# Optimization experiments

Hardware: AMD Instinct MI355X
Metric: run time of the kernel (lower is better)

Reference implementation:

```python
import jax, jax.numpy as jnp
import numpy as np

D_MODEL = 1024
H = 16
D_K = D_MODEL // H
D_FF = 4096
EPS = 1e-6
NEG = -1.0e9


def setup_inputs() -> dict:
    key = jax.random.key(0)
    ks = jax.random.split(key, 8)
    B, S = 4, 2048
    x = jax.random.normal(ks[0], (B, S, D_MODEL), dtype=jnp.float32)
    src_mask = jnp.ones((B, 1, S, S), dtype=jnp.int32)
    s = 0.02
    wq = jax.random.normal(ks[1], (D_MODEL, D_MODEL), jnp.float32) * s
    wk = jax.random.normal(ks[2], (D_MODEL, D_MODEL), jnp.float32) * s
    wv = jax.random.normal(ks[3], (D_MODEL, D_MODEL), jnp.float32) * s
    wo = jax.random.normal(ks[4], (D_MODEL, D_MODEL), jnp.float32) * s
    w1 = jax.random.normal(ks[5], (D_MODEL, D_FF), jnp.float32) * s
    b1 = jnp.zeros((D_FF,), jnp.float32)
    w2 = jax.random.normal(ks[6], (D_FF, D_MODEL), jnp.float32) * s
    b2 = jnp.zeros((D_MODEL,), jnp.float32)
    # LayerNorm params are scalars in the original (torch.ones(1)/zeros(1))
    a1 = jnp.ones((1,), jnp.float32); bt1 = jnp.zeros((1,), jnp.float32)
    a2 = jnp.ones((1,), jnp.float32); bt2 = jnp.zeros((1,), jnp.float32)
    return {"x": x, "src_mask": src_mask, "wq": wq, "wk": wk, "wv": wv,
            "wo": wo, "w1": w1, "b1": b1, "w2": w2, "b2": b2,
            "a1": a1, "bt1": bt1, "a2": a2, "bt2": bt2}


def _layernorm(x, alpha, beta):
    # Original: (x - mean) / (std + eps), std with Bessel correction (torch default)
    mean = jnp.mean(x, axis=-1, keepdims=True)
    std = jnp.std(x, axis=-1, keepdims=True, ddof=1)
    return alpha * (x - mean) / (std + EPS) + beta


def _mha(x, mask, wq, wk, wv, wo):
    B, S, _ = x.shape
    q = (x @ wq).reshape(B, S, H, D_K).transpose(0, 2, 1, 3)  # [B,H,S,Dk]
    k = (x @ wk).reshape(B, S, H, D_K).transpose(0, 2, 1, 3)
    v = (x @ wv).reshape(B, S, H, D_K).transpose(0, 2, 1, 3)
    scores = jnp.einsum('bhqd,bhkd->bhqk', q, k) / jnp.sqrt(jnp.float32(D_K))
    scores = jnp.where(mask == 0, NEG, scores)
    attn = jax.nn.softmax(scores, axis=-1)
    out = jnp.einsum('bhqk,bhkd->bhqd', attn, v)  # [B,H,S,Dk]
    out = out.transpose(0, 2, 1, 3).reshape(B, S, D_MODEL)
    return out @ wo


def reference(x, src_mask, wq, wk, wv, wo, w1, b1, w2, b2, a1, bt1, a2, bt2):
    # Sublayer 1: self-attention with post-norm residual (dropout = eval/identity)
    attn_out = _mha(x, src_mask, wq, wk, wv, wo)
    x = _layernorm(x + attn_out, a1, bt1)
    # Sublayer 2: FFN with post-norm residual
    ffn_out = jax.nn.relu(x @ w1 + b1) @ w2 + b2
    x = _layernorm(x + ffn_out, a2, bt2)
    return x
```

## Files before the change

### kernel.cpp

```cpp
#include <hip/hip_runtime.h>
#include <stdint.h>

typedef __bf16 bf16x8 __attribute__((ext_vector_type(8)));
typedef float f32x4 __attribute__((ext_vector_type(4)));
typedef unsigned short u16;
typedef u16 u16x8 __attribute__((ext_vector_type(8)));
typedef u16 u16x4 __attribute__((ext_vector_type(4)));
typedef uint32_t u32;

#define DEV __device__ __forceinline__
#define MFMA(a, b, c) __builtin_amdgcn_mfma_f32_16x16x32_bf16(a, b, c, 0, 0, 0)

static constexpr int B_ = 4, S_ = 2048, M_ = 8192, D_ = 1024, H_ = 16, DFF_ = 4096;

DEV u16 f2bf(float f) {
    union { float f; u32 u; } c; c.f = f;
    u32 u = c.u;
    return (u16)((u + 0x7fffu + ((u >> 16) & 1u)) >> 16);
}

DEV u32 cvt_pk_bf16(float lo, float hi) {
    u32 r;
    asm("v_cvt_pk_bf16_f32 %0, %1, %2" : "=v"(r) : "v"(lo), "v"(hi));
    return r;
}

DEV float v_exp2(float x) {
    float r;
    asm("v_exp_f32 %0, %1" : "=v"(r) : "v"(x));
    return r;
}

DEV void gload16(void* lds, const void* g) {
    __builtin_amdgcn_global_load_lds(
        (const __attribute__((address_space(1))) unsigned int*)g,
        (__attribute__((address_space(3))) unsigned int*)lds, 16, 0, 0);
}


__global__ __launch_bounds__(256) void k_pack_mask(const int* __restrict__ m,
                                                   u32* __restrict__ bits, int nwords) {
    int w = blockIdx.x * 256 + threadIdx.x;
    if (w >= nwords) return;
    const int4* s = (const int4*)(m + (size_t)w * 32);
    u32 r = 0;
#pragma unroll
    for (int j = 0; j < 8; j++) {
        int4 v = s[j];
        r |= (u32)(v.x != 0) << (j * 4) | (u32)(v.y != 0) << (j * 4 + 1) |
             (u32)(v.z != 0) << (j * 4 + 2) | (u32)(v.w != 0) << (j * 4 + 3);
    }
    bits[w] = r;
}

__global__ __launch_bounds__(256) void k_cast_bf16(const float* __restrict__ s,
                                                   u16* __restrict__ d, int n4) {
    int i = blockIdx.x * 256 + threadIdx.x;
    if (i >= n4) return;
    f32x4 v = ((const f32x4*)s)[i];
    u16x4 o;
    o[0] = f2bf(v[0]); o[1] = f2bf(v[1]); o[2] = f2bf(v[2]); o[3] = f2bf(v[3]);
    ((u16x4*)d)[i] = o;
}

__global__ void k_transpose_cast(const float* __restrict__ s, u16* __restrict__ d,
                                 int K, int N) {
    __shared__ float t[32][33];
    int n0 = blockIdx.x * 32, k0 = blockIdx.y * 32;
    int tx = threadIdx.x, ty = threadIdx.y;
#pragma unroll
    for (int i = 0; i < 4; i++)
        t[ty + i * 8][tx] = s[(size_t)(k0 + ty + i * 8) * N + n0 + tx];
    __syncthreads();
#pragma unroll
    for (int i = 0; i < 4; i++)
        d[(size_t)(n0 + ty + i * 8) * K + k0 + tx] = f2bf(t[tx][ty + i * 8]);
}

template <int EPI>
__global__ __launch_bounds__(512, 4) void k_gemm8(const u16* __restrict__ A,
                                                  const u16* __restrict__ Bt,
                                                  float* __restrict__ Cf,
                                                  u16* __restrict__ Cb,
                                                  const float* __restrict__ bias,
                                                  const float* __restrict__ resid,
                                                  u16* __restrict__ Vt,
                                                  int N, int K) {
    __shared__ u16 As[2][128 * 64];
    __shared__ u16 Bs[2][128 * 64];
    const int tid = threadIdx.x, lane = tid & 63, wave = tid >> 6;
    const int lr = lane & 15, lg = lane >> 4;
    const int wm = wave >> 1, wn = wave & 1;
    const int nbx = N >> 7;
    const int chunk = gridDim.x >> 3;
    const int id = ((int)blockIdx.x & 7) * chunk + ((int)blockIdx.x >> 3);
    const size_t row0 = (size_t)(id / nbx) * 128;
    const int col0 = (id % nbx) * 128;
    const int srow = lane >> 3;
    const int sgr = (lane & 7) ^ srow;
    const int NT = K >> 6;
    f32x4 acc[2][4] = {};

    auto stage = [&](int buf, int t) {
#pragma unroll
        for (int i = 0; i < 2; i++) {
            int c = i * 8 + wave;
            gload16((char*)&As[buf][0] + c * 1024,
                    (const char*)(A + (row0 + c * 8 + srow) * K + t * 64 + sgr * 8));
        }
#pragma unroll
        for (int i = 0; i < 2; i++) {
            int c = i * 8 + wave;
            gload16((char*)&Bs[buf][0] + c * 1024,
                    (const char*)(Bt + (size_t)(col0 + c * 8 + srow) * K + t * 64 + sgr * 8));
        }
    };

    stage(0, 0);
    for (int t = 0; t < NT; ++t) {
        const int cur = t & 1;
        if (t + 1 < NT) {
            stage(cur ^ 1, t + 1);
            asm volatile("s_waitcnt vmcnt(4)" ::: "memory");
        } else {
            asm volatile("s_waitcnt vmcnt(0)" ::: "memory");
        }
        __builtin_amdgcn_s_barrier();
        asm volatile("" ::: "memory");
        bf16x8 bF[4][2];
#pragma unroll
        for (int n = 0; n < 4; n++) {
            int r = wn * 64 + n * 16 + lr;
            int rb = r * 128, sw = (r & 7) << 4;
#pragma unroll
            for (int ks = 0; ks < 2; ks++)
                bF[n][ks] = *(const bf16x8*)((char*)&Bs[cur][0] +
                                             (rb + ((ks * 64 + lg * 16) ^ sw)));
        }
#pragma unroll
        for (int m = 0; m < 2; m++) {
            int r = wm * 32 + m * 16 + lr;
            int rb = r * 128, sw = (r & 7) << 4;
            bf16x8 a0 = *(const bf16x8*)((char*)&As[cur][0] + (rb + ((lg * 16) ^ sw)));
            bf16x8 a1 = *(const bf16x8*)((char*)&As[cur][0] + (rb + ((64 + lg * 16) ^ sw)));
            __builtin_amdgcn_s_setprio(1);
#pragma unroll
            for (int n = 0; n < 4; n++) {
                acc[m][n] = MFMA(a0, bF[n][0], acc[m][n]);
                acc[m][n] = MFMA(a1, bF[n][1], acc[m][n]);
            }
            __builtin_amdgcn_s_setprio(0);
        }
        asm volatile("" ::: "memory");
        __builtin_amdgcn_s_barrier();
    }
#pragma unroll
    for (int m = 0; m < 2; m++)
#pragma unroll
        for (int n = 0; n < 4; n++) {
            const int cg = col0 + wn * 64 + n * 16 + lr;
            const int rbase = (int)row0 + wm * 32 + m * 16 + lg * 4;
            if constexpr (EPI == 0) {
                const int proj = cg >> 10, hh = (cg >> 6) & 15, dk = cg & 63;
                const int b = rbase >> 11, s = rbase & 2047;
                if (proj == 2) {
                    u16x4 ov;
#pragma unroll
                    for (int i = 0; i < 4; i++) ov[i] = f2bf(acc[m][n][i]);
                    *(u16x4*)(Vt + ((size_t)(b * 16 + hh) * 64 + dk) * 2048 + s) = ov;
                } else {
                    const float sc = (proj == 0) ? 0.1803368801111832f : 1.f;
                    size_t base = ((size_t)(proj * 64 + b * 16 + hh) * 2048 + s) * 64 + dk;
#pragma unroll
                    for (int i = 0; i < 4; i++)
                        Cb[base + (size_t)i * 64] = f2bf(acc[m][n][i] * sc);
                }
            } else {
#pragma unroll
                for (int i = 0; i < 4; i++) {
                    const int rg = rbase + i;
                    float v = acc[m][n][i];
                    if constexpr (EPI == 1) {
                        Cf[(size_t)rg * N + cg] = v + resid[(size_t)rg * N + cg];
                    } else if constexpr (EPI == 2) {
                        v += bias[cg];
                        v = v > 0.f ? v : 0.f;
                        Cb[(size_t)rg * N + cg] = f2bf(v);
                    } else {
                        Cf[(size_t)rg * N + cg] = v + bias[cg] + resid[(size_t)rg * N + cg];
                    }
                }
            }
        }
}

template <int EPI>
__global__ __launch_bounds__(512, 2) void k_gemm256(const u16* __restrict__ A,
                                                    const u16* __restrict__ Bt,
                                                    float* __restrict__ Cf,
                                                    u16* __restrict__ Cb,
                                                    const float* __restrict__ bias,
                                                    int N, int K) {
    __shared__ u16 As[2][256 * 64];
    __shared__ u16 Bs[2][256 * 64];
    const int tid = threadIdx.x, lane = tid & 63, wave = tid >> 6;
    const int lr = lane & 15, lg = lane >> 4;
    const int wm = wave >> 2, wn = wave & 3;
    const int nbx = N >> 8;
    const int chunk = gridDim.x >> 3;
    const int id = ((int)blockIdx.x & 7) * chunk + ((int)blockIdx.x >> 3);
    const size_t row0 = (size_t)(id / nbx) * 256;
    const int col0 = (id % nbx) * 256;
    const int srow = lane >> 3;
    const int sgr = (lane & 7) ^ srow;
    const int NT = K >> 6;
    f32x4 acc[8][4] = {};

    auto stage_half = [&](int isB, int buf, int t, int h) {
        const u16* g = isB ? Bt : A;
        const size_t grow0 = isB ? (size_t)col0 : row0;
        char* base = isB ? (char*)&Bs[buf][0] : (char*)&As[buf][0];
#pragma unroll
        for (int l = 0; l < 2; l++) {
            int rt = h * 128 + l * 64 + wave * 8;
            gload16(base + rt * 128,
                    (const char*)(g + (grow0 + rt + srow) * K + t * 64 + sgr * 8));
        }
    };
    auto rdA = [&](int cur, int mh, int m, int kk) -> bf16x8 {
        int r = wm * 128 + mh * 64 + m * 16 + lr;
        int gi = kk * 4 + lg;
        return *(const bf16x8*)((char*)&As[cur][0] + r * 128 + ((gi ^ (r & 7)) << 4));
    };
    auto rdB = [&](int cur, int nh, int n, int kk) -> bf16x8 {
        int r = wn * 64 + nh * 32 + n * 16 + lr;
        int gi = kk * 4 + lg;
        return *(const bf16x8*)((char*)&Bs[cur][0] + r * 128 + ((gi ^ (r & 7)) << 4));
    };

    stage_half(0, 0, 0, 0); stage_half(0, 0, 0, 1);
    stage_half(1, 0, 0, 0); stage_half(1, 0, 0, 1);
    stage_half(1, 1, 1, 0); stage_half(1, 1, 1, 1);
    asm volatile("s_waitcnt vmcnt(4)" ::: "memory");
    __builtin_amdgcn_s_barrier();

    bf16x8 aF[4][2], b0F[2][2], b1F[2][2];
    for (int t = 0; t < NT; ++t) {
        const int cur = t & 1, nxt = cur ^ 1;
#pragma unroll
        for (int m = 0; m < 4; m++) { aF[m][0] = rdA(cur, 0, m, 0); aF[m][1] = rdA(cur, 0, m, 1); }
#pragma unroll
        for (int n = 0; n < 2; n++) { b0F[n][0] = rdB(cur, 0, n, 0); b0F[n][1] = rdB(cur, 0, n, 1); }
        if (t + 1 < NT) stage_half(0, nxt, t + 1, 0);
        __builtin_amdgcn_s_barrier();
        asm volatile("s_waitcnt lgkmcnt(0)" ::: "memory");
        __builtin_amdgcn_sched_barrier(0);
        __builtin_amdgcn_s_setprio(1);
#pragma unroll
        for (int m = 0; m < 4; m++)
#pragma unroll
            for (int n = 0; n < 2; n++) {
                acc[m][n] = MFMA(aF[m][0], b0F[n][0], acc[m][n]);
                acc[m][n] = MFMA(aF[m][1], b0F[n][1], acc[m][n]);
            }
        __builtin_amdgcn_s_setprio(0);
        __builtin_amdgcn_s_barrier();
#pragma unroll
        for (int n = 0; n < 2; n++) { b1F[n][0] = rdB(cur, 1, n, 0); b1F[n][1] = rdB(cur, 1, n, 1); }
        if (t + 1 < NT) stage_half(0, nxt, t + 1, 1);
        __builtin_amdgcn_s_barrier();
        asm volatile("s_waitcnt lgkmcnt(0)" ::: "memory");
        __builtin_amdgcn_sched_barrier(0);
        __builtin_amdgcn_s_setprio(1);
#pragma unroll
        for (int m = 0; m < 4; m++)
#pragma unroll
            for (int n = 0; n < 2; n++) {
                acc[m][2 + n] = MFMA(aF[m][0], b1F[n][0], acc[m][2 + n]);
                acc[m][2 + n] = MFMA(aF[m][1], b1F[n][1], acc[m][2 + n]);
            }
        __builtin_amdgcn_s_setprio(0);
        __builtin_amdgcn_s_barrier();
#pragma unroll
        for (int m = 0; m < 4; m++) { aF[m][0] = rdA(cur, 1, m, 0); aF[m][1] = rdA(cur, 1, m, 1); }
        if (t + 2 < NT) stage_half(1, cur, t + 2, 0);
        __builtin_amdgcn_s_barrier();
        asm volatile("s_waitcnt lgkmcnt(0)" ::: "memory");
        __builtin_amdgcn_sched_barrier(0);
        __builtin_amdgcn_s_setprio(1);
#pragma unroll
        for (int m = 0; m < 4; m++)
#pragma unroll
            for (int n = 0; n < 2; n++) {
                acc[4 + m][2 + n] = MFMA(aF[m][0], b1F[n][0], acc[4 + m][2 + n]);
                acc[4 + m][2 + n] = MFMA(aF[m][1], b1F[n][1], acc[4 + m][2 + n]);
            }
        __builtin_amdgcn_s_setprio(0);
        __builtin_amdgcn_s_barrier();
        if (t + 2 < NT) stage_half(1, cur, t + 2, 1);
        if (t + 1 < NT) {
            if (t + 2 < NT) asm volatile("s_waitcnt vmcnt(4)" ::: "memory");
            else            asm volatile("s_waitcnt vmcnt(0)" ::: "memory");
        }
        __builtin_amdgcn_s_barrier();
        __builtin_amdgcn_s_setprio(1);
#pragma unroll
        for (int m = 0; m < 4; m++)
#pragma unroll
            for (int n = 0; n < 2; n++) {
                acc[4 + m][n] = MFMA(aF[m][0], b0F[n][0], acc[4 + m][n]);
                acc[4 + m][n] = MFMA(aF[m][1], b0F[n][1], acc[4 + m][n]);
            }
        __builtin_amdgcn_s_setprio(0);
        __builtin_amdgcn_s_barrier();
    }
#pragma unroll
    for (int m = 0; m < 8; m++)
#pragma unroll
        for (int n = 0; n < 4; n++)
#pragma unroll
            for (int i = 0; i < 4; i++) {
                int rg = (int)row0 + wm * 128 + m * 16 + lg * 4 + i;
                int cg = col0 + wn * 64 + n * 16 + lr;
                float v = acc[m][n][i];
                if constexpr (EPI == 2) {
                    v += bias[cg];
                    v = v > 0.f ? v : 0.f;
                    Cb[(size_t)rg * N + cg] = f2bf(v);
                } else {
                    Cf[(size_t)rg * N + cg] = v;
                }
            }
}

__global__ __launch_bounds__(256) void k_attn(const u16* __restrict__ qkv,
                                              const u16* __restrict__ vT,
                                              const u32* __restrict__ mbits,
                                              u16* __restrict__ outb) {
    __shared__ u16 Kt[2][64 * 64];
    __shared__ u16 Vt[2][64 * 64];
    __shared__ u16 Pt[4][32 * 64];
    __shared__ u32 pm[2][128][2];
    const int tid = threadIdx.x, lane = tid & 63, wave = tid >> 6;
    const int lr = lane & 15, lg = lane >> 4;
    const int id0 = blockIdx.y * 16 + blockIdx.x;
    const int id = (id0 & 7) * 128 + (id0 >> 3);
    const int bh = id >> 4;
    const int b = bh >> 4, h = bh & 15;
    const int qb0 = (id & 15) * 128;
    const size_t qbase = (size_t)bh * (2048 * 64);
    const size_t kbase = (size_t)(64 + bh) * (2048 * 64);
    const size_t vtbase = (size_t)bh * (64 * 2048);

    bf16x8 qf[2][2];
    const int q0 = qb0 + wave * 32;
#pragma unroll
    for (int rs = 0; rs < 2; rs++)
#pragma unroll
        for (int kf = 0; kf < 2; kf++)
            qf[rs][kf] = *(const bf16x8*)(qkv + qbase +
                                          (size_t)(q0 + rs * 16 + lr) * 64 + kf * 32 + lg * 8);

    u16x8 ones_u;
#pragma unroll
    for (int e = 0; e < 8; e++) ones_u[e] = 0x3f80;
    const bf16x8 ones8 = *(const bf16x8*)&ones_u;

    f32x4 o[2][4] = {};
    f32x4 lacc[2] = {};
    const int str = tid >> 2, sq = tid & 3;
    const int swzs = (str & 7) << 4;
    const f32x4 zinit = {-16.f, -16.f, -16.f, -16.f};

    u16x8 krA, krB, vrA, vrB; u32 mwA;
    auto issue_loads = [&](int kv0n) {
        const u16* ksrc = qkv + kbase + (size_t)(kv0n + str) * 64 + sq * 16;
        krA = *(const u16x8*)ksrc; krB = *(const u16x8*)(ksrc + 8);
        const u16* vsrc = vT + vtbase + (size_t)str * 2048 + kv0n + sq * 16;
        vrA = *(const u16x8*)vsrc; vrB = *(const u16x8*)(vsrc + 8);
        mwA = mbits[(size_t)(b * 2048 + qb0 + (tid >> 1)) * 64 + (kv0n >> 5) + (tid & 1)];
    };
    auto write_tile = [&](int buf) -> bool {
        int b0 = str * 128 + sq * 32;
        *(u16x8*)((char*)&Kt[buf][0] + ((b0) ^ swzs)) = krA;
        *(u16x8*)((char*)&Kt[buf][0] + ((b0 + 16) ^ swzs)) = krB;
        *(u16x8*)((char*)&Vt[buf][0] + ((b0) ^ swzs)) = vrA;
        *(u16x8*)((char*)&Vt[buf][0] + ((b0 + 16) ^ swzs)) = vrB;
        pm[buf][tid >> 1][tid & 1] = mwA;
        return (__ballot(mwA == 0xffffffffu) == ~0ull);
    };

    issue_loads(0);
    bool aon_nxt = write_tile(0);
    for (int t = 0; t < 32; ++t) {
        const int cur = t & 1;
        const bool aon_cur = aon_nxt;
        if (t + 1 < 32) issue_loads((t + 1) * 64);
        asm volatile("s_waitcnt lgkmcnt(0)" ::: "memory");
        __builtin_amdgcn_s_barrier();

        f32x4 st[2][4];
#pragma unroll
        for (int ks = 0; ks < 4; ks++) {
            int rr = ks * 16 + lr;
            int rb = rr * 128, sw = (rr & 7) << 4;
            bf16x8 k0 = *(const bf16x8*)((char*)&Kt[cur][0] + ((rb + lg * 16) ^ sw));
            bf16x8 k1 = *(const bf16x8*)((char*)&Kt[cur][0] + ((rb + 64 + lg * 16) ^ sw));
#pragma unroll
            for (int rs = 0; rs < 2; rs++) {
                f32x4 z = MFMA(k0, qf[rs][0], zinit);
                z = MFMA(k1, qf[rs][1], z);
                st[rs][ks] = z;
            }
        }
        if (!aon_cur) {
#pragma unroll
            for (int rs = 0; rs < 2; rs++) {
                u32 w0 = pm[cur][wave * 32 + rs * 16 + lr][0];
                u32 w1 = pm[cur][wave * 32 + rs * 16 + lr][1];
#pragma unroll
                for (int ks = 0; ks < 4; ks++)
#pragma unroll
                    for (int i = 0; i < 4; i++) {
                        int kv = ks * 16 + lg * 4 + i;
                        u32 w = (kv & 32) ? w1 : w0;
                        if (!((w >> (kv & 31)) & 1u)) st[rs][ks][i] = -1e9f;
                    }
            }
        }
#pragma unroll
        for (int rs = 0; rs < 2; rs++) {
            int prow = rs * 16 + lr;
            int pb = prow * 128, swp = (prow & 7) << 4;
#pragma unroll
            for (int ks = 0; ks < 4; ks++) {
                uint2 w;
                w.x = cvt_pk_bf16(v_exp2(st[rs][ks][0]), v_exp2(st[rs][ks][1]));
                w.y = cvt_pk_bf16(v_exp2(st[rs][ks][2]), v_exp2(st[rs][ks][3]));
                *(uint2*)((char*)&Pt[wave][0] + ((pb + ks * 32 + lg * 8) ^ swp)) = w;
            }
        }
        asm volatile("s_waitcnt lgkmcnt(0)" ::: "memory");
        __builtin_amdgcn_sched_barrier(0);
        bf16x8 pf[2][2];
#pragma unroll
        for (int rs = 0; rs < 2; rs++) {
            int prow = rs * 16 + lr;
            int pb = prow * 128, swp = (prow & 7) << 4;
            pf[rs][0] = *(const bf16x8*)((char*)&Pt[wave][0] + ((pb + lg * 16) ^ swp));
            pf[rs][1] = *(const bf16x8*)((char*)&Pt[wave][0] + ((pb + 64 + lg * 16) ^ swp));
        }
#pragma unroll
        for (int rs = 0; rs < 2; rs++) {
            lacc[rs] = MFMA(ones8, pf[rs][0], lacc[rs]);
            lacc[rs] = MFMA(ones8, pf[rs][1], lacc[rs]);
        }
#pragma unroll
        for (int ns = 0; ns < 4; ns++) {
            int vr = ns * 16 + lr;
            int vb = vr * 128, sw = (vr & 7) << 4;
            bf16x8 v0 = *(const bf16x8*)((char*)&Vt[cur][0] + ((vb + lg * 16) ^ sw));
            bf16x8 v1 = *(const bf16x8*)((char*)&Vt[cur][0] + ((vb + 64 + lg * 16) ^ sw));
#pragma unroll
            for (int rs = 0; rs < 2; rs++) {
                o[rs][ns] = MFMA(v0, pf[rs][0], o[rs][ns]);
                o[rs][ns] = MFMA(v1, pf[rs][1], o[rs][ns]);
            }
        }
        if (t + 1 < 32) aon_nxt = write_tile(cur ^ 1);
    }
#pragma unroll
    for (int rs = 0; rs < 2; rs++) {
        float inv = 1.f / lacc[rs][0];
        int qg = qb0 + wave * 32 + rs * 16 + lr;
#pragma unroll
        for (int ns = 0; ns < 4; ns++) {
            u16x4 ov;
#pragma unroll
            for (int i = 0; i < 4; i++) ov[i] = f2bf(o[rs][ns][i] * inv);
            *(u16x4*)(outb + (size_t)(b * 2048 + qg) * 1024 + h * 64 + ns * 16 + lg * 4) = ov;
        }
    }
}

template <bool WB>
__global__ __launch_bounds__(256) void k_ln(const float* __restrict__ tin,
                                            float* __restrict__ outf,
                                            u16* __restrict__ outb,
                                            const float* __restrict__ alpha,
                                            const float* __restrict__ beta) {
    const int row = blockIdx.x, tid = threadIdx.x;
    const f32x4 t = ((const f32x4*)(tin + (size_t)row * 1024))[tid];
    float s = t[0] + t[1] + t[2] + t[3];
    float ss = t[0] * t[0] + t[1] * t[1] + t[2] * t[2] + t[3] * t[3];
#pragma unroll
    for (int m2 = 1; m2 < 64; m2 <<= 1) {
        s += __shfl_xor(s, m2);
        ss += __shfl_xor(ss, m2);
    }
    __shared__ float ps[4], pss[4];
    if ((tid & 63) == 0) { ps[tid >> 6] = s; pss[tid >> 6] = ss; }
    __syncthreads();
    s = ps[0] + ps[1] + ps[2] + ps[3];
    ss = pss[0] + pss[1] + pss[2] + pss[3];
    const float mean = s * (1.f / 1024.f);
    float var = (ss - 1024.f * mean * mean) * (1.f / 1023.f);
    var = fmaxf(var, 0.f);
    const float inv = alpha[0] / (sqrtf(var) + 1e-6f);
    const float bet = beta[0];
    f32x4 oo;
#pragma unroll
    for (int i = 0; i < 4; i++) oo[i] = (t[i] - mean) * inv + bet;
    ((f32x4*)(outf + (size_t)row * 1024))[tid] = oo;
    if constexpr (WB) {
        u16x4 ob;
#pragma unroll
        for (int i = 0; i < 4; i++) ob[i] = f2bf(oo[i]);
        ((u16x4*)(outb + (size_t)row * 1024))[tid] = ob;
    }
}

extern "C" void kernel_launch(void* const* d_in, const int* in_sizes, int n_in,
                              void* d_out, int out_size, void* d_ws, size_t ws_size,
                              hipStream_t stream) {
    const float* x   = (const float*)d_in[0];
    const int*   msk = (const int*)d_in[1];
    const float* wq  = (const float*)d_in[2];
    const float* wk  = (const float*)d_in[3];
    const float* wv  = (const float*)d_in[4];
    const float* wo  = (const float*)d_in[5];
    const float* w1  = (const float*)d_in[6];
    const float* b1  = (const float*)d_in[7];
    const float* w2  = (const float*)d_in[8];
    const float* b2  = (const float*)d_in[9];
    const float* a1  = (const float*)d_in[10];
    const float* bt1 = (const float*)d_in[11];
    const float* a2  = (const float*)d_in[12];
    const float* bt2 = (const float*)d_in[13];
    float* out = (float*)d_out;

    char* ws = (char*)d_ws;
    size_t off = 0;
    auto alloc = [&](size_t bytes) {
        void* p = ws + off;
        off += (bytes + 255) & ~(size_t)255;
        return p;
    };
    u16* xb    = (u16*)alloc((size_t)M_ * D_ * 2);
    u16* wqkvT = (u16*)alloc((size_t)3 * D_ * D_ * 2);
    u16* woT   = (u16*)alloc((size_t)D_ * D_ * 2);
    u16* w1T   = (u16*)alloc((size_t)DFF_ * D_ * 2);
    u16* w2T   = (u16*)alloc((size_t)D_ * DFF_ * 2);
    u32* mbits = (u32*)alloc((size_t)B_ * S_ * 64 * 4);
    u16* aout  = (u16*)alloc((size_t)M_ * D_ * 2);
    float* y   = (float*)alloc((size_t)M_ * D_ * 4);
    float* x1  = (float*)alloc((size_t)M_ * D_ * 4);
    u16* x1b   = (u16*)alloc((size_t)M_ * D_ * 2);
    u16* vTb   = (u16*)alloc((size_t)64 * 64 * 2048 * 2);
    u16* qkv   = (u16*)alloc((size_t)M_ * DFF_ * 2);
    u16* hft   = qkv;

    k_pack_mask<<<dim3((B_ * S_ * 64) / 256), 256, 0, stream>>>(msk, mbits, B_ * S_ * 64);
    k_cast_bf16<<<dim3((M_ * D_ / 4) / 256), 256, 0, stream>>>(x, xb, M_ * D_ / 4);
    dim3 tb(32, 8);
    k_transpose_cast<<<dim3(32, 32), tb, 0, stream>>>(wq, wqkvT, D_, D_);
    k_transpose_cast<<<dim3(32, 32), tb, 0, stream>>>(wk, wqkvT + D_ * D_, D_, D_);
    k_transpose_cast<<<dim3(32, 32), tb, 0, stream>>>(wv, wqkvT + 2 * D_ * D_, D_, D_);
    k_transpose_cast<<<dim3(32, 32), tb, 0, stream>>>(wo, woT, D_, D_);
    k_transpose_cast<<<dim3(128, 32), tb, 0, stream>>>(w1, w1T, D_, DFF_);
    k_transpose_cast<<<dim3(32, 128), tb, 0, stream>>>(w2, w2T, DFF_, D_);

    k_gemm8<0><<<dim3(1536), 512, 0, stream>>>(xb, wqkvT, nullptr, qkv, nullptr,
                                               nullptr, vTb, 3 * D_, D_);
    k_attn<<<dim3(16, 64), 256, 0, stream>>>(qkv, vTb, mbits, aout);
    k_gemm8<1><<<dim3(512), 512, 0, stream>>>(aout, woT, y, nullptr, nullptr, x,
                                              nullptr, D_, D_);
    k_ln<true><<<dim3(M_), 256, 0, stream>>>(y, x1, x1b, a1, bt1);
    k_gemm256<2><<<dim3(512), 512, 0, stream>>>(x1b, w1T, nullptr, hft, b1, DFF_, D_);
    k_gemm8<3><<<dim3(512), 512, 0, stream>>>(hft, w2T, y, nullptr, b2, x1,
                                              nullptr, D_, DFF_);
    k_ln<false><<<dim3(M_), 256, 0, stream>>>(y, out, nullptr, a2, bt2);
}
```

Baseline: 412.7 us.

## Use 32x32x16 MFMA in attention and keep P in registers via permlane swap

The attention kernel switches from 16x16x32 MFMA tiles to 32x32x16 tiles, so each wave computes a 32-query by 64-key score block with fewer, larger MFMAs. The softmax probabilities are repacked directly in registers using v_permlane32_swap into the A-operand layout for the PV product, which removes the per-wave shared-memory P round trip and its waitcnt. The mask bits and output indexing are remapped to the new accumulator layout. Output stores become scalar 2-byte writes per lane instead of 4-element vectors, which may cost some store efficiency.

```diff
diff --git a/kernel.cpp b/kernel.cpp
--- a/kernel.cpp
+++ b/kernel.cpp
@@ -3,6 +3,7 @@
 
 typedef __bf16 bf16x8 __attribute__((ext_vector_type(8)));
 typedef float f32x4 __attribute__((ext_vector_type(4)));
+typedef float f32x16 __attribute__((ext_vector_type(16)));
 typedef unsigned short u16;
 typedef u16 u16x8 __attribute__((ext_vector_type(8)));
 typedef u16 u16x4 __attribute__((ext_vector_type(4)));
@@ -10,6 +11,7 @@
 
 #define DEV __device__ __forceinline__
 #define MFMA(a, b, c) __builtin_amdgcn_mfma_f32_16x16x32_bf16(a, b, c, 0, 0, 0)
+#define MFMA32(a, b, c) __builtin_amdgcn_mfma_f32_32x32x16_bf16(a, b, c, 0, 0, 0)
 
 static constexpr int B_ = 4, S_ = 2048, M_ = 8192, D_ = 1024, H_ = 16, DFF_ = 4096;
 
@@ -339,10 +341,9 @@
                                               u16* __restrict__ outb) {
     __shared__ u16 Kt[2][64 * 64];
     __shared__ u16 Vt[2][64 * 64];
-    __shared__ u16 Pt[4][32 * 64];
     __shared__ u32 pm[2][128][2];
     const int tid = threadIdx.x, lane = tid & 63, wave = tid >> 6;
-    const int lr = lane & 15, lg = lane >> 4;
+    const int l31 = lane & 31, hi = lane >> 5;
     const int id0 = blockIdx.y * 16 + blockIdx.x;
     const int id = (id0 & 7) * 128 + (id0 >> 3);
     const int bh = id >> 4;
@@ -352,25 +353,25 @@
     const size_t kbase = (size_t)(64 + bh) * (2048 * 64);
     const size_t vtbase = (size_t)bh * (64 * 2048);
 
-    bf16x8 qf[2][2];
+    bf16x8 qf[4];
     const int q0 = qb0 + wave * 32;
 #pragma unroll
-    for (int rs = 0; rs < 2; rs++)
-#pragma unroll
-        for (int kf = 0; kf < 2; kf++)
-            qf[rs][kf] = *(const bf16x8*)(qkv + qbase +
-                                          (size_t)(q0 + rs * 16 + lr) * 64 + kf * 32 + lg * 8);
+    for (int dstep = 0; dstep < 4; dstep++)
+        qf[dstep] = *(const bf16x8*)(qkv + qbase + (size_t)(q0 + l31) * 64 +
+                                     dstep * 16 + hi * 8);
 
     u16x8 ones_u;
 #pragma unroll
     for (int e = 0; e < 8; e++) ones_u[e] = 0x3f80;
     const bf16x8 ones8 = *(const bf16x8*)&ones_u;
 
-    f32x4 o[2][4] = {};
-    f32x4 lacc[2] = {};
+    f32x16 o0 = {}, o1 = {}, lacc = {};
+    f32x16 zin;
+#pragma unroll
+    for (int r = 0; r < 16; r++) zin[r] = -16.f;
+
     const int str = tid >> 2, sq = tid & 3;
     const int swzs = (str & 7) << 4;
-    const f32x4 zinit = {-16.f, -16.f, -16.f, -16.f};
 
     u16x8 krA, krB, vrA, vrB; u32 mwA;
     auto issue_loads = [&](int kv0n) {
@@ -399,87 +400,72 @@
         asm volatile("s_waitcnt lgkmcnt(0)" ::: "memory");
         __builtin_amdgcn_s_barrier();
 
-        f32x4 st[2][4];
+        u32 mw0 = 0xffffffffu, mw1 = 0xffffffffu;
+        if (!aon_cur) {
+            mw0 = pm[cur][wave * 32 + l31][0] >> (hi * 4);
+            mw1 = pm[cur][wave * 32 + l31][1] >> (hi * 4);
+        }
+
+        bf16x8 pa[4];
+#pragma unroll
+        for (int kvb = 0; kvb < 2; kvb++) {
+            f32x16 st = zin;
+#pragma unroll
+            for (int dstep = 0; dstep < 4; dstep++) {
+                int r = kvb * 32 + l31;
+                bf16x8 kf = *(const bf16x8*)((char*)&Kt[cur][0] + r * 128 +
+                                             ((dstep * 32 + hi * 16) ^ ((r & 7) << 4)));
+                st = MFMA32(kf, qf[dstep], st);
+            }
+            if (!aon_cur) {
+                u32 w = kvb ? mw1 : mw0;
+#pragma unroll
+                for (int r = 0; r < 16; r++) {
+                    int sh = (r & 3) + 8 * (r >> 2);
+                    if (!((w >> sh) & 1u)) st[r] = -1e9f;
+                }
+            }
+#pragma unroll
+            for (int r = 0; r < 16; r++) st[r] = v_exp2(st[r]);
+            u32 wA[4], wB[4];
+#pragma unroll
+            for (int g = 0; g < 4; g++) {
+                wA[g] = cvt_pk_bf16(st[4 * g], st[4 * g + 1]);
+                wB[g] = cvt_pk_bf16(st[4 * g + 2], st[4 * g + 3]);
+            }
+#pragma unroll
+            for (int s = 0; s < 2; s++) {
+                u32 xA = wA[2 * s], yA = wA[2 * s + 1];
+                asm("v_permlane32_swap_b32 %0, %1" : "+v"(xA), "+v"(yA));
+                u32 xB = wB[2 * s], yB = wB[2 * s + 1];
+                asm("v_permlane32_swap_b32 %0, %1" : "+v"(xB), "+v"(yB));
+                union { u32 w[4]; bf16x8 v; } pk;
+                pk.w[0] = xA; pk.w[1] = xB; pk.w[2] = yA; pk.w[3] = yB;
+                pa[kvb * 2 + s] = pk.v;
+            }
+        }
+#pragma unroll
+        for (int ks = 0; ks < 4; ks++) lacc = MFMA32(pa[ks], ones8, lacc);
 #pragma unroll
         for (int ks = 0; ks < 4; ks++) {
-            int rr = ks * 16 + lr;
-            int rb = rr * 128, sw = (rr & 7) << 4;
-            bf16x8 k0 = *(const bf16x8*)((char*)&Kt[cur][0] + ((rb + lg * 16) ^ sw));
-            bf16x8 k1 = *(const bf16x8*)((char*)&Kt[cur][0] + ((rb + 64 + lg * 16) ^ sw));
-#pragma unroll
-            for (int rs = 0; rs < 2; rs++) {
-                f32x4 z = MFMA(k0, qf[rs][0], zinit);
-                z = MFMA(k1, qf[rs][1], z);
-                st[rs][ks] = z;
-            }
-        }
-        if (!aon_cur) {
-#pragma unroll
-            for (int rs = 0; rs < 2; rs++) {
-                u32 w0 = pm[cur][wave * 32 + rs * 16 + lr][0];
-                u32 w1 = pm[cur][wave * 32 + rs * 16 + lr][1];
-#pragma unroll
-                for (int ks = 0; ks < 4; ks++)
-#pragma unroll
-                    for (int i = 0; i < 4; i++) {
-                        int kv = ks * 16 + lg * 4 + i;
-                        u32 w = (kv & 32) ? w1 : w0;
-                        if (!((w >> (kv & 31)) & 1u)) st[rs][ks][i] = -1e9f;
-                    }
-            }
-        }
-#pragma unroll
-        for (int rs = 0; rs < 2; rs++) {
-            int prow = rs * 16 + lr;
-            int pb = prow * 128, swp = (prow & 7) << 4;
-#pragma unroll
-            for (int ks = 0; ks < 4; ks++) {
-                uint2 w;
-                w.x = cvt_pk_bf16(v_exp2(st[rs][ks][0]), v_exp2(st[rs][ks][1]));
-                w.y = cvt_pk_bf16(v_exp2(st[rs][ks][2]), v_exp2(st[rs][ks][3]));
-                *(uint2*)((char*)&Pt[wave][0] + ((pb + ks * 32 + lg * 8) ^ swp)) = w;
-            }
-        }
-        asm volatile("s_waitcnt lgkmcnt(0)" ::: "memory");
-        __builtin_amdgcn_sched_barrier(0);
-        bf16x8 pf[2][2];
-#pragma unroll
-        for (int rs = 0; rs < 2; rs++) {
-            int prow = rs * 16 + lr;
-            int pb = prow * 128, swp = (prow & 7) << 4;
-            pf[rs][0] = *(const bf16x8*)((char*)&Pt[wave][0] + ((pb + lg * 16) ^ swp));
-            pf[rs][1] = *(const bf16x8*)((char*)&Pt[wave][0] + ((pb + 64 + lg * 16) ^ swp));
-        }
-#pragma unroll
-        for (int rs = 0; rs < 2; rs++) {
-            lacc[rs] = MFMA(ones8, pf[rs][0], lacc[rs]);
-            lacc[rs] = MFMA(ones8, pf[rs][1], lacc[rs]);
-        }
-#pragma unroll
-        for (int ns = 0; ns < 4; ns++) {
-            int vr = ns * 16 + lr;
-            int vb = vr * 128, sw = (vr & 7) << 4;
-            bf16x8 v0 = *(const bf16x8*)((char*)&Vt[cur][0] + ((vb + lg * 16) ^ sw));
-            bf16x8 v1 = *(const bf16x8*)((char*)&Vt[cur][0] + ((vb + 64 + lg * 16) ^ sw));
-#pragma unroll
-            for (int rs = 0; rs < 2; rs++) {
-                o[rs][ns] = MFMA(v0, pf[rs][0], o[rs][ns]);
-                o[rs][ns] = MFMA(v1, pf[rs][1], o[rs][ns]);
-            }
+            int r0 = l31;
+            bf16x8 vb0 = *(const bf16x8*)((char*)&Vt[cur][0] + r0 * 128 +
+                                          ((ks * 32 + hi * 16) ^ ((r0 & 7) << 4)));
+            int r1 = 32 + l31;
+            bf16x8 vb1 = *(const bf16x8*)((char*)&Vt[cur][0] + r1 * 128 +
+                                          ((ks * 32 + hi * 16) ^ ((r1 & 7) << 4)));
+            o0 = MFMA32(pa[ks], vb0, o0);
+            o1 = MFMA32(pa[ks], vb1, o1);
         }
         if (t + 1 < 32) aon_nxt = write_tile(cur ^ 1);
     }
 #pragma unroll
-    for (int rs = 0; rs < 2; rs++) {
-        float inv = 1.f / lacc[rs][0];
-        int qg = qb0 + wave * 32 + rs * 16 + lr;
-#pragma unroll
-        for (int ns = 0; ns < 4; ns++) {
-            u16x4 ov;
-#pragma unroll
-            for (int i = 0; i < 4; i++) ov[i] = f2bf(o[rs][ns][i] * inv);
-            *(u16x4*)(outb + (size_t)(b * 2048 + qg) * 1024 + h * 64 + ns * 16 + lg * 4) = ov;
-        }
+    for (int r = 0; r < 16; r++) {
+        float inv = 1.f / lacc[r];
+        int qg = qb0 + wave * 32 + (r & 3) + 8 * (r >> 2) + 4 * hi;
+        size_t rowb = (size_t)(b * 2048 + qg) * 1024 + h * 64 + l31;
+        outb[rowb] = f2bf(o0[r] * inv);
+        outb[rowb + 32] = f2bf(o1[r] * inv);
     }
 }
 
```

After: 425.4 us. 1.03x slower.
